# Performance work log

Hardware: AMD Instinct MI355X
Metric: run time of the kernel (lower is better)

## Reference

```python
import jax, jax.numpy as jnp
import numpy as np

NUM_USERS = 100000
NUM_ITEMS = 200000
D = 128          # embedding_dim
K = 4            # num interest heads
B = 4096
H = 256          # history length
H1, H2 = 512, 256  # hidden_units


def setup_inputs() -> dict:
    key = jax.random.key(0)
    ks = jax.random.split(key, 10)
    inp = {
        "user_ids": jax.random.randint(ks[0], (B,), 0, NUM_USERS),
        "candidate_items": jax.random.randint(ks[1], (B,), 0, NUM_ITEMS),
        "history_items": jax.random.randint(ks[2], (B, H), 0, NUM_ITEMS),
        "item_table": jax.random.normal(ks[3], (NUM_ITEMS, D), dtype=jnp.float32) * 0.05,
        "Wp": jax.random.normal(ks[4], (D, K), dtype=jnp.float32) * (1.0 / np.sqrt(D)),
        "W1": jax.random.normal(ks[5], (2 * D, H1), dtype=jnp.float32) * (1.0 / np.sqrt(2 * D)),
        "b1": jnp.zeros((H1,), dtype=jnp.float32),
        "W2": jax.random.normal(ks[6], (H1, H2), dtype=jnp.float32) * (1.0 / np.sqrt(H1)),
        "b2": jnp.zeros((H2,), dtype=jnp.float32),
        "W3": jax.random.normal(ks[7], (H2, 1), dtype=jnp.float32) * (1.0 / np.sqrt(H2)),
        "b3": jnp.zeros((1,), dtype=jnp.float32),
    }
    return inp


def reference(user_ids, candidate_items, history_items, item_table, Wp,
              W1, b1, W2, b2, W3, b3):
    # user_ids is unused by the original forward (user_emb never applied)
    item_vecs = item_table[history_items]          # (B, H, D)
    cand_vec = item_table[candidate_items]         # (B, D)

    # per-interest attention scores, softmax over history axis
    scores = jnp.einsum('bhd,dk->bhk', item_vecs, Wp)   # (B, H, K)
    scores = jax.nn.softmax(scores, axis=1)

    # softmax-weighted pooling -> K interest vectors per user
    interest_vectors = jnp.einsum('bhk,bhd->bkd', scores, item_vecs)  # (B, K, D)

    # similarity to candidate, pick best interest (data-dependent gather)
    sim_scores = jnp.einsum('bkd,bd->bk', interest_vectors, cand_vec)  # (B, K)
    best_idx = jnp.argmax(sim_scores, axis=-1)                          # (B,)
    selected = jnp.take_along_axis(
        interest_vectors, best_idx[:, None, None], axis=1)[:, 0, :]    # (B, D)

    # MLP tail: [2D -> 512] ReLU [512 -> 256] ReLU [256 -> 1], sigmoid
    x = jnp.concatenate([selected, cand_vec], axis=-1)  # (B, 2D)
    x = jax.nn.relu(x @ W1 + b1)
    x = jax.nn.relu(x @ W2 + b2)
    out = (x @ W3 + b3)[:, 0]                            # (B,)
    return jax.nn.sigmoid(out)
```

## Files before the change

kernel.cpp:

```cpp
#include <hip/hip_runtime.h>
#include <hip/hip_bf16.h>
#include <math.h>

#define B_SZ   4096
#define H_LEN  256
#define D_DIM  128
#define K_HEADS 4
#define H1_DIM 512
#define H2_DIM 256

#define CH     32
#define NCH    8
#define TPAD   132

typedef __attribute__((ext_vector_type(8))) short bf16x8;
typedef __attribute__((ext_vector_type(4))) float f32x4;

__global__ __launch_bounds__(256, 7) void interest_kernel(
    const int*   __restrict__ cand_ids,
    const int*   __restrict__ hist,
    const float* __restrict__ table,
    const float* __restrict__ Wp,
    __hip_bfloat16* __restrict__ Xbf)
{
    __shared__ float tile[CH * TPAD];
    __shared__ float wpt[K_HEADS * D_DIM];
    __shared__ float exps4[CH * 4];
    __shared__ float candv[D_DIM];
    __shared__ int   rowids[H_LEN];
    __shared__ float lsumW[16];
    __shared__ float simred[4][K_HEADS];
    __shared__ int   bestk;

    const int b    = blockIdx.x;
    const int t    = threadIdx.x;
    const int lane = t & 63, w = t >> 6;
    const int r    = t >> 3, q = t & 7;
    const int d    = t & 127, half = t >> 7;

    if (t < D_DIM) {
        float4 w4 = ((const float4*)Wp)[t];
        wpt[0 * D_DIM + t] = w4.x;
        wpt[1 * D_DIM + t] = w4.y;
        wpt[2 * D_DIM + t] = w4.z;
        wpt[3 * D_DIM + t] = w4.w;
    }
    const int cand = cand_ids[b];
    if (t >= 128 && t < 160) {
        int c = t - 128;
        ((float4*)candv)[c] = ((const float4*)(table + (long long)cand * D_DIM))[c];
    }
    rowids[t] = hist[(long long)b * H_LEN + t];

    __syncthreads();

    float a0 = 0.f, a1 = 0.f, a2 = 0.f, a3 = 0.f;
    float l0 = 0.f, l1 = 0.f, l2 = 0.f, l3 = 0.f;

    for (int c = 0; c < NCH; ++c) {
        const int   row = rowids[(c << 5) + r];
        const float* rp = table + (long long)row * D_DIM + (q << 2);
        float4 v0 = *(const float4*)(rp + 0 * 32);
        float4 v1 = *(const float4*)(rp + 1 * 32);
        float4 v2 = *(const float4*)(rp + 2 * 32);
        float4 v3 = *(const float4*)(rp + 3 * 32);

        float s0 = 0.f, s1 = 0.f, s2 = 0.f, s3 = 0.f;
        float4 va;
        #define DO_J(JJ, VV)                                                    \
        {   va = VV;                                                            \
            const int cb = (q << 2) + (JJ << 5);                                \
            float4 w0 = *(const float4*)(wpt + 0 * D_DIM + cb);                 \
            float4 w1 = *(const float4*)(wpt + 1 * D_DIM + cb);                 \
            float4 w2 = *(const float4*)(wpt + 2 * D_DIM + cb);                 \
            float4 w3 = *(const float4*)(wpt + 3 * D_DIM + cb);                 \
            s0 += va.x * w0.x + va.y * w0.y + va.z * w0.z + va.w * w0.w;        \
            s1 += va.x * w1.x + va.y * w1.y + va.z * w1.z + va.w * w1.w;        \
            s2 += va.x * w2.x + va.y * w2.y + va.z * w2.z + va.w * w2.w;        \
            s3 += va.x * w3.x + va.y * w3.y + va.z * w3.z + va.w * w3.w;        \
            *(float4*)(tile + r * TPAD + cb) = va;                              \
        }
        DO_J(0, v0) DO_J(1, v1) DO_J(2, v2) DO_J(3, v3)
        #undef DO_J

        s0 += __shfl_xor(s0, 1); s0 += __shfl_xor(s0, 2); s0 += __shfl_xor(s0, 4);
        s1 += __shfl_xor(s1, 1); s1 += __shfl_xor(s1, 2); s1 += __shfl_xor(s1, 4);
        s2 += __shfl_xor(s2, 1); s2 += __shfl_xor(s2, 2); s2 += __shfl_xor(s2, 4);
        s3 += __shfl_xor(s3, 1); s3 += __shfl_xor(s3, 2); s3 += __shfl_xor(s3, 4);

        float e0 = expf(s0), e1 = expf(s1), e2 = expf(s2), e3 = expf(s3);
        if (q == 0) ((float4*)exps4)[r] = make_float4(e0, e1, e2, e3);

        float t0 = e0, t1 = e1, t2 = e2, t3 = e3;
        #pragma unroll
        for (int off = 8; off <= 32; off <<= 1) {
            t0 += __shfl_xor(t0, off);
            t1 += __shfl_xor(t1, off);
            t2 += __shfl_xor(t2, off);
            t3 += __shfl_xor(t3, off);
        }
        l0 += t0; l1 += t1; l2 += t2; l3 += t3;

        __syncthreads();

        #pragma unroll
        for (int i = 0; i < 16; ++i) {
            int hl = (half << 4) + i;
            float4 e4 = ((const float4*)exps4)[hl];
            float  vv = tile[hl * TPAD + d];
            a0 += e4.x * vv; a1 += e4.y * vv; a2 += e4.z * vv; a3 += e4.w * vv;
        }

        __syncthreads();
    }

    float* partBp = tile;
    float* ivbufp = tile + 512;

    if (half == 1) ((float4*)partBp)[d] = make_float4(a0, a1, a2, a3);
    if (lane == 0) ((float4*)lsumW)[w]  = make_float4(l0, l1, l2, l3);
    __syncthreads();

    float s0 = 0.f, s1 = 0.f, s2 = 0.f, s3 = 0.f;
    if (half == 0) {
        float4 pb = ((const float4*)partBp)[d];
        float4 L0 = ((const float4*)lsumW)[0];
        float4 L1 = ((const float4*)lsumW)[1];
        float4 L2 = ((const float4*)lsumW)[2];
        float4 L3 = ((const float4*)lsumW)[3];
        float i0 = 1.f / (L0.x + L1.x + L2.x + L3.x);
        float i1 = 1.f / (L0.y + L1.y + L2.y + L3.y);
        float i2 = 1.f / (L0.z + L1.z + L2.z + L3.z);
        float i3 = 1.f / (L0.w + L1.w + L2.w + L3.w);
        a0 = (a0 + pb.x) * i0;
        a1 = (a1 + pb.y) * i1;
        a2 = (a2 + pb.z) * i2;
        a3 = (a3 + pb.w) * i3;
        ((float4*)ivbufp)[d] = make_float4(a0, a1, a2, a3);
        float cd = candv[d];
        s0 = a0 * cd; s1 = a1 * cd; s2 = a2 * cd; s3 = a3 * cd;
    }
    #pragma unroll
    for (int off = 32; off >= 1; off >>= 1) {
        s0 += __shfl_xor(s0, off);
        s1 += __shfl_xor(s1, off);
        s2 += __shfl_xor(s2, off);
        s3 += __shfl_xor(s3, off);
    }
    if (lane == 0) {
        simred[w][0] = s0; simred[w][1] = s1;
        simred[w][2] = s2; simred[w][3] = s3;
    }
    __syncthreads();

    if (t == 0) {
        float sim[4];
        #pragma unroll
        for (int k = 0; k < 4; ++k)
            sim[k] = simred[0][k] + simred[1][k] + simred[2][k] + simred[3][k];
        int best = 0;
        #pragma unroll
        for (int k = 1; k < 4; ++k) if (sim[k] > sim[best]) best = k;
        bestk = best;
    }
    __syncthreads();

    __hip_bfloat16* xrow = Xbf + (long long)b * (2 * D_DIM);
    if (t < 128) xrow[t] = __float2bfloat16(ivbufp[t * 4 + bestk]);
    else         xrow[t] = __float2bfloat16(candv[t - 128]);
}

__global__ __launch_bounds__(256) void convert_weights(
    const float* __restrict__ W1, const float* __restrict__ W2,
    __hip_bfloat16* __restrict__ W1t, __hip_bfloat16* __restrict__ W2t)
{
    __shared__ float tl[32][33];
    int bid = blockIdx.x;
    const float* W; __hip_bfloat16* Wt; int K, N;
    if (bid < 128) { W = W1; Wt = W1t; K = 2 * D_DIM; N = H1_DIM; }
    else           { W = W2; Wt = W2t; K = H1_DIM;    N = H2_DIM; bid -= 128; }
    const int ntn = N >> 5;
    const int k0 = (bid / ntn) << 5, n0 = (bid % ntn) << 5;
    const int tx = threadIdx.x & 31, ty = threadIdx.x >> 5;
    #pragma unroll
    for (int j = 0; j < 4; ++j)
        tl[ty + 8 * j][tx] = W[(long long)(k0 + ty + 8 * j) * N + n0 + tx];
    __syncthreads();
    #pragma unroll
    for (int j = 0; j < 4; ++j)
        Wt[(long long)(n0 + ty + 8 * j) * K + k0 + tx] =
            __float2bfloat16(tl[tx][ty + 8 * j]);
}

__global__ __launch_bounds__(512) void mlp_fused(
    const __hip_bfloat16* __restrict__ X,
    const __hip_bfloat16* __restrict__ W1t,
    const float* __restrict__ b1,
    const __hip_bfloat16* __restrict__ W2t,
    const float* __restrict__ b2,
    const float* __restrict__ W3,
    const float* __restrict__ b3,
    float*       __restrict__ out)
{
    __shared__ __hip_bfloat16 h1[16][H1_DIM + 8];
    __shared__ float          h2[16][H2_DIM + 4];

    const int t    = threadIdx.x;
    const int wave = t >> 6, lane = t & 63;
    const int lm   = lane & 15, quad = lane >> 4;
    const int m0   = blockIdx.x * 16;

    const __hip_bfloat16* Ap = X + (long long)(m0 + lm) * (2 * D_DIM) + quad * 8;
    bf16x8 af[8];
    #pragma unroll
    for (int it = 0; it < 8; ++it) af[it] = *(const bf16x8*)(Ap + it * 32);

    #pragma unroll
    for (int tn = 0; tn < 4; ++tn) {
        const int n0 = (wave * 4 + tn) * 16;
        const __hip_bfloat16* Bp = W1t + (long long)(n0 + lm) * (2 * D_DIM) + quad * 8;
        f32x4 acc = {0.f, 0.f, 0.f, 0.f};
        #pragma unroll
        for (int it = 0; it < 8; ++it) {
            bf16x8 bfr = *(const bf16x8*)(Bp + it * 32);
            acc = __builtin_amdgcn_mfma_f32_16x16x32_bf16(af[it], bfr, acc, 0, 0, 0);
        }
        const float bv = b1[n0 + lm];
        #pragma unroll
        for (int i = 0; i < 4; ++i)
            h1[quad * 4 + i][n0 + lm] = __float2bfloat16(fmaxf(acc[i] + bv, 0.f));
    }
    __syncthreads();

    bf16x8 a2[16];
    #pragma unroll
    for (int it = 0; it < 16; ++it)
        a2[it] = *(const bf16x8*)(&h1[lm][quad * 8 + it * 32]);

    #pragma unroll
    for (int tn = 0; tn < 2; ++tn) {
        const int n0 = (wave * 2 + tn) * 16;
        const __hip_bfloat16* Bp = W2t + (long long)(n0 + lm) * H1_DIM + quad * 8;
        f32x4 acc = {0.f, 0.f, 0.f, 0.f};
        #pragma unroll
        for (int it = 0; it < 16; ++it) {
            bf16x8 bfr = *(const bf16x8*)(Bp + it * 32);
            acc = __builtin_amdgcn_mfma_f32_16x16x32_bf16(a2[it], bfr, acc, 0, 0, 0);
        }
        const float bv = b2[n0 + lm];
        #pragma unroll
        for (int i = 0; i < 4; ++i)
            h2[quad * 4 + i][n0 + lm] = fmaxf(acc[i] + bv, 0.f);
    }
    __syncthreads();

    {
        const int row = t >> 5, c = (t & 31) * 8;
        float s = 0.f;
        #pragma unroll
        for (int j = 0; j < 8; ++j) s += h2[row][c + j] * W3[c + j];
        #pragma unroll
        for (int off = 1; off <= 16; off <<= 1) s += __shfl_xor(s, off);
        if ((lane & 31) == 0)
            out[m0 + row] = 1.f / (1.f + expf(-(s + b3[0])));
    }
}

extern "C" void kernel_launch(void* const* d_in, const int* in_sizes, int n_in,
                              void* d_out, int out_size, void* d_ws, size_t ws_size,
                              hipStream_t stream) {
    const int*   cand  = (const int*)  d_in[1];
    const int*   hist  = (const int*)  d_in[2];
    const float* table = (const float*)d_in[3];
    const float* Wp    = (const float*)d_in[4];
    const float* W1    = (const float*)d_in[5];
    const float* b1    = (const float*)d_in[6];
    const float* W2    = (const float*)d_in[7];
    const float* b2    = (const float*)d_in[8];
    const float* W3    = (const float*)d_in[9];
    const float* b3    = (const float*)d_in[10];
    float* out = (float*)d_out;

    char* p = (char*)d_ws;
    __hip_bfloat16* Xbf = (__hip_bfloat16*)p;  p += (size_t)B_SZ * 2 * D_DIM * 2;
    __hip_bfloat16* W1t = (__hip_bfloat16*)p;  p += (size_t)H1_DIM * 2 * D_DIM * 2;
    __hip_bfloat16* W2t = (__hip_bfloat16*)p;

    convert_weights<<<256, 256, 0, stream>>>(W1, W2, W1t, W2t);
    interest_kernel<<<B_SZ, 256, 0, stream>>>(cand, hist, table, Wp, Xbf);
    mlp_fused<<<B_SZ / 16, 512, 0, stream>>>(Xbf, W1t, b1, W2t, b2, W3, b3, out);
}
```

Baseline: 282.0 us.

## Prefetch next history chunk into registers and use LDS-only barriers

Software-pipelines the gather loop: the next chunk's embedding rows are loaded into registers while the current chunk is scored and pooled, so global-load latency overlaps with compute. Barriers inside the loop become a wait on LDS counters plus s_barrier, which avoids waiting on outstanding global loads. Launch bounds drop from 7 to 6 blocks per SM to make room for the extra registers, which may reduce occupancy.

After: 260.8 us. 1.08x faster.

```diff
diff --git a/kernel.cpp b/kernel.cpp
--- a/kernel.cpp
+++ b/kernel.cpp
@@ -16,7 +16,12 @@
 typedef __attribute__((ext_vector_type(8))) short bf16x8;
 typedef __attribute__((ext_vector_type(4))) float f32x4;
 
-__global__ __launch_bounds__(256, 7) void interest_kernel(
+#define LDS_BARRIER() do {                                   \
+    asm volatile("s_waitcnt lgkmcnt(0)" ::: "memory");       \
+    __builtin_amdgcn_s_barrier();                            \
+} while (0)
+
+__global__ __launch_bounds__(256, 6) void interest_kernel(
     const int*   __restrict__ cand_ids,
     const int*   __restrict__ hist,
     const float* __restrict__ table,
@@ -52,18 +57,31 @@
     }
     rowids[t] = hist[(long long)b * H_LEN + t];
 
-    __syncthreads();
+    float4 v0, v1, v2, v3;
+    {
+        const int row0 = hist[(long long)b * H_LEN + r];
+        const float* rp = table + (long long)row0 * D_DIM + (q << 2);
+        v0 = *(const float4*)(rp + 0 * 32);
+        v1 = *(const float4*)(rp + 1 * 32);
+        v2 = *(const float4*)(rp + 2 * 32);
+        v3 = *(const float4*)(rp + 3 * 32);
+    }
+
+    LDS_BARRIER();
 
     float a0 = 0.f, a1 = 0.f, a2 = 0.f, a3 = 0.f;
     float l0 = 0.f, l1 = 0.f, l2 = 0.f, l3 = 0.f;
 
     for (int c = 0; c < NCH; ++c) {
-        const int   row = rowids[(c << 5) + r];
-        const float* rp = table + (long long)row * D_DIM + (q << 2);
-        float4 v0 = *(const float4*)(rp + 0 * 32);
-        float4 v1 = *(const float4*)(rp + 1 * 32);
-        float4 v2 = *(const float4*)(rp + 2 * 32);
-        float4 v3 = *(const float4*)(rp + 3 * 32);
+        float4 u0, u1, u2, u3;
+        if (c + 1 < NCH) {
+            const int row = rowids[((c + 1) << 5) + r];
+            const float* rp = table + (long long)row * D_DIM + (q << 2);
+            u0 = *(const float4*)(rp + 0 * 32);
+            u1 = *(const float4*)(rp + 1 * 32);
+            u2 = *(const float4*)(rp + 2 * 32);
+            u3 = *(const float4*)(rp + 3 * 32);
+        }
 
         float s0 = 0.f, s1 = 0.f, s2 = 0.f, s3 = 0.f;
         float4 va;
@@ -101,7 +119,7 @@
         }
         l0 += t0; l1 += t1; l2 += t2; l3 += t3;
 
-        __syncthreads();
+        LDS_BARRIER();
 
         #pragma unroll
         for (int i = 0; i < 16; ++i) {
@@ -111,9 +129,12 @@
             a0 += e4.x * vv; a1 += e4.y * vv; a2 += e4.z * vv; a3 += e4.w * vv;
         }
 
-        __syncthreads();
-    }
-
+        LDS_BARRIER();
+
+        if (c + 1 < NCH) { v0 = u0; v1 = u1; v2 = u2; v3 = u3; }
+    }
+
+    __syncthreads();
     float* partBp = tile;
     float* ivbufp = tile + 512;
 
```
